# Kernel optimization log

Hardware: AMD Instinct MI355X
Metric: run time of the kernel (lower is better)

Reference implementation:

```python
import jax, jax.numpy as jnp
import numpy as np
from itertools import combinations

WIRES, LAYERS, CUTOFF, OUT_WIRES, BATCH = 4, 2, 10, 3, 2048

def _annih(c):
    # annihilation operator a in the Fock basis, truncated to cutoff c
    return jnp.diag(jnp.sqrt(jnp.arange(1, c, dtype=jnp.float32)), 1).astype(jnp.complex64)

_expm = jnp.vectorize(jax.scipy.linalg.expm, signature='(n,n)->(n,n)')

def _squeeze(r, phi, a):
    # S(z) = exp((z* a^2 - z a+^2)/2), z = r e^{i phi}; r, phi have arbitrary batch shape
    z = (r * jnp.exp(1j * phi)).astype(jnp.complex64)[..., None, None]
    a2 = a @ a
    ad2 = a.conj().T @ a.conj().T
    return _expm(0.5 * (jnp.conj(z) * a2 - z * ad2))

def _disp(r, phi, a):
    # D(alpha) = exp(alpha a+ - alpha* a), alpha = r e^{i phi}
    al = (r * jnp.exp(1j * phi)).astype(jnp.complex64)[..., None, None]
    ad = a.conj().T
    return _expm(al * ad - jnp.conj(al) * a)

def _bs(theta, phi, a):
    # SF BSgate: B = exp(theta (e^{i phi} a b+ - e^{-i phi} a+ b))
    ad = a.conj().T
    G = theta * (jnp.exp(1j * phi) * jnp.kron(a, ad) - jnp.exp(-1j * phi) * jnp.kron(ad, a))
    return jax.scipy.linalg.expm(G.astype(jnp.complex64))

def _cx(s, a):
    # SF CXgate: exp(-i s x1 p2 / hbar) = exp(-(s/2) (a+a+) kron (b-b+)) with hbar=2
    ad = a.conj().T
    G = (-s / 2.0) * jnp.kron(a + ad, a - ad)
    return jax.scipy.linalg.expm(G.astype(jnp.complex64))

def _apply1(state, U, m):
    # apply single-mode gate U ([c,c] shared or [B,c,c] per-sample) to mode m
    if U.ndim == 2:
        return jnp.moveaxis(jnp.tensordot(state, U, axes=[[1 + m], [1]]), -1, 1 + m)
    st = jnp.moveaxis(state, 1 + m, -1)
    st = jnp.einsum('b...j,bij->b...i', st, U)
    return jnp.moveaxis(st, -1, 1 + m)

def _apply2(state, U4, m1, m2):
    # apply two-mode gate U4 [c,c,c,c] (out1,out2,in1,in2) to modes (m1, m2)
    st = jnp.moveaxis(state, (1 + m1, 1 + m2), (-2, -1))
    st = jnp.einsum('b...kl,ijkl->b...ij', st, U4)
    return jnp.moveaxis(st, (-2, -1), (1 + m1, 1 + m2))

def _forward(jets, s_scale, disp_mag, disp_phase, squeeze_mag, squeeze_phase, w_dense, b_dense):
    B, c = jets.shape[0], CUTOFF
    a = _annih(c)
    eta, phi, pt = jets[:, :, 0], jets[:, :, 1], jets[:, :, 2]  # each [B, WIRES]
    scale = 10.0 / (1.0 + jnp.exp(-s_scale)) + 0.01
    # vacuum |0...0> for every sample
    state = jnp.zeros((B,) + (c,) * WIRES, jnp.complex64)
    state = state.at[(slice(None),) + (0,) * WIRES].set(1.0)
    # per-sample data-encoding gates
    S_enc = _squeeze(eta, pt * phi / 2.0, a)      # [B, WIRES, c, c]
    D_enc = _disp(scale * pt, eta, a)             # [B, WIRES, c, c]
    for w in range(WIRES):
        state = _apply1(state, S_enc[:, w], w)
        state = _apply1(state, D_enc[:, w], w)
    # fixed entangling gates (shared across batch)
    CX = _cx(1.0, a).reshape(c, c, c, c)
    BS = _bs(jnp.pi / 4.0, jnp.pi / 2.0, a).reshape(c, c, c, c)
    # learned per-layer single-mode gates (shared across batch)
    S_lay = _squeeze(squeeze_mag, squeeze_phase, a)  # [LAYERS, WIRES, c, c]
    D_lay = _disp(disp_mag, disp_phase, a)
    for L in range(LAYERS):
        for (i, j) in combinations(range(WIRES), 2):
            state = _apply2(state, CX, i, j)
        for i in range(WIRES):
            state = _apply2(state, BS, i, (i + 1) % WIRES)
        for w in range(WIRES):
            state = _apply1(state, S_lay[L, w], w)
            state = _apply1(state, D_lay[L, w], w)
    probs = jnp.abs(state) ** 2
    nvec = jnp.arange(c, dtype=jnp.float32)
    photons = jnp.stack(
        [probs.sum(axis=tuple(1 + k for k in range(WIRES) if k != m)) @ nvec
         for m in range(OUT_WIRES)], axis=1)  # [B, OUT_WIRES] mean photon numbers
    return (photons @ w_dense + b_dense)[:, 0]  # [B]

def setup_inputs() -> dict:
    key = jax.random.key(0)
    ks = jax.random.split(key, 8)
    u = lambda k, sh: jax.random.uniform(k, sh, jnp.float32, -1.0, 1.0)
    return {
        'jets': 0.3 * jax.random.normal(ks[0], (BATCH, WIRES, 3), jnp.float32),
        's_scale': u(ks[1], ()),
        'disp_mag': u(ks[2], (LAYERS, WIRES)),
        'disp_phase': u(ks[3], (LAYERS, WIRES)),
        'squeeze_mag': u(ks[4], (LAYERS, WIRES)),
        'squeeze_phase': u(ks[5], (LAYERS, WIRES)),
        'w_dense': u(ks[6], (OUT_WIRES, 1)),
        'b_dense': jnp.zeros((1,), jnp.float32),
    }

def reference(jets, s_scale, disp_mag, disp_phase, squeeze_mag, squeeze_phase, w_dense, b_dense):
    return _forward(jets, s_scale, disp_mag, disp_phase, squeeze_mag, squeeze_phase, w_dense, b_dense)
```

## Files before the change

### kernel.cpp

```cpp
#include <hip/hip_runtime.h>
#include <math.h>


namespace {

constexpr int NTB = 1024;
constexpr int SMEM_STATE = 162352;
constexpr double THETA = 0.7853981633974483096;

struct cxf { float x, y; };
typedef float v2f __attribute__((ext_vector_type(2)));
typedef float v4f __attribute__((ext_vector_type(4)));

constexpr int U_OFF = 15872;

__device__ __forceinline__ cxf gen_squeeze_f(int i, int j, float zr, float zi){
  if (j == i+2){ float g = 0.5f*sqrtf((float)((i+1)*(i+2))); return {zr*g, -zi*g}; }
  if (i == j+2){ float g = 0.5f*sqrtf((float)((j+1)*(j+2))); return {-zr*g, -zi*g}; }
  return {0.f, 0.f};
}
__device__ __forceinline__ cxf gen_disp_f(int i, int j, float ar, float ai){
  if (i == j+1){ float g = sqrtf((float)i); return {ar*g, ai*g}; }
  if (j == i+1){ float g = sqrtf((float)j); return {-ar*g, ai*g}; }
  return {0.f, 0.f};
}

__device__ void expm_f32(bool act, int n, cxf* M, cxf* P, cxf* T, cxf* R, int lane){
  const int n2 = n*n;
  if (act){
    for (int e=lane; e<n2; e+=64){ M[e].x *= 0x1p-10f; M[e].y *= 0x1p-10f; }
    for (int e=lane; e<n2; e+=64){
      P[e] = M[e];
      cxf r = M[e];
      if (e % (n+1) == 0) r.x += 1.f;
      R[e] = r;
    }
  }
  __syncthreads();
  for (int t=2; t<=12; ++t){
    if (act){
      float inv = 1.f/(float)t;
      for (int e=lane; e<n2; e+=64){
        int i = e/n, j = e - i*n;
        float ax=0.f, ay=0.f;
        for (int k=0;k<n;k++){
          cxf p = P[i*n+k], m = M[k*n+j];
          ax += p.x*m.x - p.y*m.y;
          ay += p.x*m.y + p.y*m.x;
        }
        T[e] = {ax*inv, ay*inv};
      }
    }
    __syncthreads();
    { cxf* tmp = P; P = T; T = tmp; }
    if (act){ for (int e=lane; e<n2; e+=64){ R[e].x += P[e].x; R[e].y += P[e].y; } }
    __syncthreads();
  }
  for (int s=0; s<10; ++s){
    if (act){
      for (int e=lane; e<n2; e+=64){
        int i = e/n, j = e - i*n;
        float ax=0.f, ay=0.f;
        for (int k=0;k<n;k++){
          cxf p = R[i*n+k], q = R[k*n+j];
          ax += p.x*q.x - p.y*q.y;
          ay += p.x*q.y + p.y*q.x;
        }
        T[e] = {ax, ay};
      }
    }
    __syncthreads();
    { cxf* tmp = R; R = T; T = tmp; }
    __syncthreads();
  }
}

__global__ __launch_bounds__(256)
void gates_kernel(const float* __restrict__ dmag, const float* __restrict__ dphase,
                  const float* __restrict__ smag, const float* __restrict__ sphase,
                  float* __restrict__ wsf){
  __shared__ double lam[10];
  __shared__ float scr[4][4][200];
  const int tid = threadIdx.x;
  const int wv = tid >> 6, lane = tid & 63, g = blockIdx.x;
  float* ws_V  = wsf;
  float* ws_VT = wsf + 100;
  float* ws_W  = wsf + 200;
  cxf* ws_BS   = (cxf*)(wsf + 1200);
  cxf* ws_stage= (cxf*)(wsf + 6600);

  if (tid < 10){
    double lo = -6.0, hi = 6.0;
    for (int it=0; it<80; ++it){
      double mid = 0.5*(lo+hi);
      int cnt = 0; double q = 1.0;
      for (int i=0;i<10;i++){
        q = -mid - (i ? (double)i/q : 0.0);
        if (fabs(q) < 1e-300) q = -1e-300;
        if (q < 0.0) cnt++;
      }
      if (cnt > tid) hi = mid; else lo = mid;
    }
    double x = 0.5*(lo+hi);
    double p[10];
    p[0] = 1.0; p[1] = x;
    for (int k=1;k<9;k++) p[k+1] = (x*p[k] - sqrt((double)k)*p[k-1]) * (1.0/sqrt((double)(k+1)));
    double nn=0.0; for (int k=0;k<10;k++) nn += p[k]*p[k];
    double inv = 1.0/sqrt(nn);
    lam[tid] = x;
    if (g == 0){
      for (int k=0;k<10;k++){
        float v = (float)(p[k]*inv);
        ws_V[k*10+tid]  = v;
        ws_VT[tid*10+k] = v;
      }
    }
  }
  __syncthreads();

  int t = g*4 + wv;
  bool act = (t < 45);
  int n = 10, bn = 0, ilo = 0;
  if (act && t >= 10 && t < 29){
    bn = t - 10; ilo = bn < 10 ? 0 : bn - 9;
    int ihi = bn < 10 ? bn : 9;
    n = ihi - ilo + 1;
  }
  cxf* M = (cxf*)scr[wv][0];
  cxf* P = (cxf*)scr[wv][1];
  cxf* T = (cxf*)scr[wv][2];
  cxf* R = (cxf*)scr[wv][3];
  if (act){
    if (t < 10){
      float l = (float)lam[t];
      for (int e=lane; e<100; e+=64){
        int i=e/10, j=e-10*i;
        float v = 0.f;
        if (j == i+1) v = -0.5f*l*sqrtf((float)(i+1));
        else if (i == j+1) v = 0.5f*l*sqrtf((float)i);
        M[e] = {v, 0.f};
      }
    } else if (t < 29){
      for (int e=lane; e<n*n; e+=64){
        int rr=e/n, c=e-n*rr;
        float v = 0.f;
        if (c == rr+1) v = (float)THETA*sqrtf((float)((ilo+rr+1)*(bn-ilo-rr)));
        else if (rr == c+1) v = (float)THETA*sqrtf((float)((ilo+c+1)*(bn-ilo-c)));
        M[e] = {0.f, v};
      }
    } else {
      int idx = t-29, kind = idx>>3, L=(idx>>2)&1, w=idx&3;
      float r_ = kind ? dmag[L*4+w]   : smag[L*4+w];
      float ph = kind ? dphase[L*4+w] : sphase[L*4+w];
      float zr = r_*cosf(ph), zi = r_*sinf(ph);
      for (int e=lane; e<100; e+=64){
        int i=e/10, j=e-10*i;
        M[e] = kind ? gen_disp_f(i,j,zr,zi) : gen_squeeze_f(i,j,zr,zi);
      }
    }
  }
  __syncthreads();
  expm_f32(act, n, M, P, T, R, lane);
  if (act){
    if (t < 10){
      for (int e=lane;e<100;e+=64){
        int i=e/10, j=e-10*i;
        ws_W[t*100 + j*10 + i] = R[e].x;
      }
    } else if (t < 29){
      for (int e=lane;e<100;e+=64){
        int rr=e/10, c=e-10*rr;
        cxf o; o.x=0.f; o.y=0.f;
        if (rr < n && c < n) o = R[rr*n+c];
        ws_BS[bn*100 + c*10 + rr] = o;
      }
    } else {
      int idx = t-29;
      for (int e=lane;e<100;e+=64) ws_stage[idx*100 + e] = R[e];
    }
  }
}

__global__ __launch_bounds__(512)
void fuse_kernel(float* __restrict__ wsf){
  __shared__ cxf ulraw[8][100];
  const int tid = threadIdx.x, wv = tid>>6, lane = tid&63;
  const cxf* stage = (const cxf*)(wsf + 6600);
  cxf* ws_UL = (cxf*)(wsf + 5000);
  cxf* ws_WU = (cxf*)(wsf + 9800);
  const float* V  = wsf;
  const float* Wt = wsf + 200;
  const cxf* Sm = stage + wv*100;
  const cxf* Dm = stage + (8+wv)*100;
  for (int e=lane; e<100; e+=64){
    int i=e/10, j=e-10*i;
    float ax=0.f, ay=0.f;
    for (int k=0;k<10;k++){
      cxf d=Dm[i*10+k], s=Sm[k*10+j];
      ax += d.x*s.x - d.y*s.y;
      ay += d.x*s.y + d.y*s.x;
    }
    ulraw[wv][e] = {ax, ay};
  }
  __syncthreads();
  cxf t0={0.f,0.f}, t1={0.f,0.f};
  if (wv == 0){
    {
      int e=lane, i=e/10, j=e-10*i;
      float ox=0.f, oy=0.f;
      for (int k=0;k<10;k++){ float v=V[k*10+i]; ox+=v*ulraw[0][k*10+j].x; oy+=v*ulraw[0][k*10+j].y; }
      t0 = {ox, oy};
    }
    if (lane+64 < 100){
      int e=lane+64, i=e/10, j=e-10*i;
      float ox=0.f, oy=0.f;
      for (int k=0;k<10;k++){ float v=V[k*10+i]; ox+=v*ulraw[0][k*10+j].x; oy+=v*ulraw[0][k*10+j].y; }
      t1 = {ox, oy};
    }
  }
  __syncthreads();
  if (wv == 0){
    ulraw[0][lane] = t0;
    if (lane+64 < 100) ulraw[0][lane+64] = t1;
  }
  __syncthreads();
  for (int e=tid; e<400; e+=512){
    int fi = e/100, r = e-100*fi;
    int f = (fi==0) ? 0 : (3+fi);
    int i=r/10, j=r-10*i;
    ws_UL[f*100 + j*10 + i] = ulraw[f][i*10+j];
  }
  for (int round=0; round<4; ++round){
    int id = round*8 + wv;
    if (id < 30){
      int b = 1 + id/10, n = id - (id/10)*10;
      const cxf* Ub = ulraw[b];
      for (int e=lane; e<100; e+=64){
        int i=e/10, j=e-10*i;
        float ax=0.f, ay=0.f;
        for (int k=0;k<10;k++){
          float w = Wt[n*100 + k*10 + i];
          ax += w*Ub[k*10+j].x;
          ay += w*Ub[k*10+j].y;
        }
        cxf o; o.x=ax; o.y=ay;
        ws_WU[id*100 + j*10 + i] = o;
      }
    }
  }
}

__global__ __launch_bounds__(128)
void enc_kernel(const float* __restrict__ jets, const float* __restrict__ sscale,
                float* __restrict__ wsf){
  __shared__ float scr[2][4][200];
  __shared__ cxf col[10];
  __shared__ cxf uacc[10];
  const int tid = threadIdx.x, wv = tid>>6, lane = tid&63;
  const int blk = blockIdx.x, b = blk>>2, w = blk&3;

  float eta = jets[b*12 + w*3 + 0];
  float jph = jets[b*12 + w*3 + 1];
  float pt  = jets[b*12 + w*3 + 2];

  cxf* M = (cxf*)scr[wv][0];
  cxf* P = (cxf*)scr[wv][1];
  cxf* T = (cxf*)scr[wv][2];
  cxf* R = (cxf*)scr[wv][3];
  {
    float zr, zi;
    if (wv == 0){ float phs = pt*jph*0.5f; zr = eta*cosf(phs); zi = eta*sinf(phs); }
    else {
      double sc = 10.0/(1.0 + exp(-(double)sscale[0])) + 0.01;
      float mag = (float)sc*pt; zr = mag*cosf(eta); zi = mag*sinf(eta);
    }
    for (int e=lane; e<100; e+=64){
      int i=e/10, j=e-10*i;
      M[e] = wv ? gen_disp_f(i,j,zr,zi) : gen_squeeze_f(i,j,zr,zi);
    }
  }
  __syncthreads();
  expm_f32(true, 10, M, P, T, R, lane);
  cxf* Rs = (cxf*)scr[0][3];
  cxf* Rd = (cxf*)scr[1][3];
  if (tid < 10) col[tid] = Rs[tid*10];
  __syncthreads();
  if (tid < 10){
    float ax=0.f, ay=0.f;
    for (int k=0;k<10;k++){
      cxf d = Rd[tid*10+k], c = col[k];
      ax += d.x*c.x - d.y*c.y;
      ay += d.x*c.y + d.y*c.x;
    }
    uacc[tid] = {ax, ay};
  }
  __syncthreads();
  if (tid < 10){
    float rx, ry;
    if (w == 0){
      rx = 0.f; ry = 0.f;
      for (int k=0;k<10;k++){
        float v = wsf[k*10 + tid];
        rx += v*uacc[k].x;
        ry += v*uacc[k].y;
      }
    } else { rx = uacc[tid].x; ry = uacc[tid].y; }
    float* u_out = wsf + U_OFF + (b*40 + w*10 + tid)*2;
    u_out[0] = rx;
    u_out[1] = ry;
  }
}

__device__ __forceinline__ constexpr int WS(int w){
  return w==0 ? 1010 : (w==1 ? 101 : (w==2 ? 10 : 1));
}

#define DECL_ACC4 \
  v4f a0={0.f,0.f,0.f,0.f}, a1=a0, a2=a0, a3=a0, a4=a0, \
      a5=a0, a6=a0, a7=a0, a8=a0, a9=a0;

#define LDS_RD10 \
  v4f r0=S[base], r1=S[base+sm], r2=S[base+2*sm], r3=S[base+3*sm], r4=S[base+4*sm], \
      r5=S[base+5*sm], r6=S[base+6*sm], r7=S[base+7*sm], r8=S[base+8*sm], r9=S[base+9*sm];

#define CE(i,ur,ui) \
  a##i = __builtin_elementwise_fma((v4f){(ur),(ur),(ur),(ur)}, vv, a##i); \
  a##i = __builtin_elementwise_fma((v4f){-(ui),(ui),-(ui),(ui)}, vs, a##i);
#define RE(i,u) a##i = __builtin_elementwise_fma((v4f){(u),(u),(u),(u)}, vv, a##i);

#define CSTEP(rk,krow) { \
  const v4f* Up = (const v4f*)(U + (krow)*10); \
  v4f q0=Up[0],q1=Up[1],q2=Up[2],q3=Up[3],q4=Up[4]; \
  v4f vv=rk, vs=__builtin_shufflevector(rk,rk,1,0,3,2); \
  CE(0,q0.x,q0.y) CE(1,q0.z,q0.w) CE(2,q1.x,q1.y) CE(3,q1.z,q1.w) \
  CE(4,q2.x,q2.y) CE(5,q2.z,q2.w) CE(6,q3.x,q3.y) CE(7,q3.z,q3.w) \
  CE(8,q4.x,q4.y) CE(9,q4.z,q4.w) }
#define CSTEP_ALL CSTEP(r0,0) CSTEP(r1,1) CSTEP(r2,2) CSTEP(r3,3) CSTEP(r4,4) \
  CSTEP(r5,5) CSTEP(r6,6) CSTEP(r7,7) CSTEP(r8,8) CSTEP(r9,9)

#define RSTEP2(ra_,rb_,krow) { \
  const v4f* Mp = (const v4f*)(Mt + (krow)*10); \
  v4f q0=Mp[0],q1=Mp[1],q2=Mp[2],q3=Mp[3],q4=Mp[4]; \
  { v4f vv=ra_; RE(0,q0.x) RE(1,q0.y) RE(2,q0.z) RE(3,q0.w) RE(4,q1.x) \
                RE(5,q1.y) RE(6,q1.z) RE(7,q1.w) RE(8,q2.x) RE(9,q2.y) } \
  { v4f vv=rb_; RE(0,q2.z) RE(1,q2.w) RE(2,q3.x) RE(3,q3.y) RE(4,q3.z) \
                RE(5,q3.w) RE(6,q4.x) RE(7,q4.y) RE(8,q4.z) RE(9,q4.w) } }
#define RSTEP_ALL RSTEP2(r0,r1,0) RSTEP2(r2,r3,2) RSTEP2(r4,r5,4) \
  RSTEP2(r6,r7,6) RSTEP2(r8,r9,8)

#define PST4(i) { S[base + (i)*sm] = a##i; }
#define PALL4 PST4(0) PST4(1) PST4(2) PST4(3) PST4(4) PST4(5) PST4(6) PST4(7) PST4(8) PST4(9)
#define BSTQ(r) if ((r) < sz){ S[wadr] = a##r; wadr += ds; }
#define BSTQ_ALL BSTQ(0) BSTQ(1) BSTQ(2) BSTQ(3) BSTQ(4) BSTQ(5) BSTQ(6) BSTQ(7) BSTQ(8) BSTQ(9)

__device__ __forceinline__ void apply1_c4(v4f* S, const cxf* __restrict__ U, int m, int tid){
  const int sm = WS(m);
  const int x0 = (m==0)?1:0, x1=(m<=1)?2:1, x2=(m<=2)?3:2;
  const int s0 = WS(x0), s1 = WS(x1), s2 = WS(x2);
  if (tid < 1000){
    int c0=tid/100, rem=tid-100*c0, c1=rem/10, c2=rem-10*c1;
    int base = c0*s0 + c1*s1 + c2*s2;
    LDS_RD10
    DECL_ACC4
    CSTEP_ALL
    PALL4
  }
}

__device__ __forceinline__ void apply1_r4(v4f* S, const float* __restrict__ Mt, int m, int tid){
  const int sm = WS(m);
  const int x0 = (m==0)?1:0, x1=(m<=1)?2:1, x2=(m<=2)?3:2;
  const int s0 = WS(x0), s1 = WS(x1), s2 = WS(x2);
  if (tid < 1000){
    int c0=tid/100, rem=tid-100*c0, c1=rem/10, c2=rem-10*c1;
    int base = c0*s0 + c1*s1 + c2*s2;
    LDS_RD10
    DECL_ACC4
    RSTEP_ALL
    PALL4
  }
}

__device__ __forceinline__ void applyW4(v4f* S, const float* __restrict__ Wall, int m1, int m2, int tid){
  const int sm  = WS(m2);
  const int sm1 = WS(m1);
  int ra=-1, rb=-1;
  for (int q=0;q<4;q++) if (q!=m1 && q!=m2){ if (ra<0) ra=q; else rb=q; }
  const int sa0 = WS(ra), sb0 = WS(rb);
  const bool sw = (sa0==101 && sb0==10);
  const int sa = sw ? sb0 : sa0, sb = sw ? sa0 : sb0;
  if (tid < 1000){
    int n = tid/100, rem = tid-100*n, qa = rem/10, qb = rem-10*qa;
    int base = n*sm1 + qa*sa + qb*sb;
    const float* __restrict__ Mt = Wall + n*100;
    LDS_RD10
    DECL_ACC4
    RSTEP_ALL
    PALL4
  }
}

__device__ __forceinline__ void applyWU4(v4f* S, const cxf* __restrict__ WUall, int m2, int tid){
  const int sm = WS(m2);
  const int ra = (m2==1)?2:1;
  const int rb = (m2==3)?2:3;
  const int sa0 = WS(ra), sb0 = WS(rb);
  const bool sw = (sa0==101 && sb0==10);
  const int sa = sw ? sb0 : sa0, sb = sw ? sa0 : sb0;
  if (tid < 1000){
    int n = tid/100, rem = tid-100*n, qa = rem/10, qb = rem-10*qa;
    int base = n*WS(0) + qa*sa + qb*sb;
    const cxf* __restrict__ U = WUall + n*100;
    LDS_RD10
    DECL_ACC4
    CSTEP_ALL
    PALL4
  }
}

__device__ __forceinline__ v2f measure14(const v4f* S, const cxf* __restrict__ U, int m, int tid){
  const int sm = WS(m);
  const int x0 = (m==0)?1:0, x1=(m<=1)?2:1, x2=3;
  const int s0 = WS(x0), s1 = WS(x1), s2 = WS(x2);
  v2f s = {0.f, 0.f};
  if (tid < 1000){
    int c0=tid/100, rem=tid-100*c0, c1=rem/10, c2=rem-10*c1;
    int base = c0*s0 + c1*s1 + c2*s2;
    LDS_RD10
    DECL_ACC4
    CSTEP_ALL
    #define MQ4(i) { s.x += (float)(i)*(a##i.x*a##i.x + a##i.y*a##i.y); \
                     s.y += (float)(i)*(a##i.z*a##i.z + a##i.w*a##i.w); }
    MQ4(1) MQ4(2) MQ4(3) MQ4(4) MQ4(5) MQ4(6) MQ4(7) MQ4(8) MQ4(9)
    #undef MQ4
  }
  return s;
}

__device__ __forceinline__ void applyBS4(v4f* S, const cxf* __restrict__ BSp, int m1, int m2, int tid){
  int ra=-1, rb=-1;
  for (int q=0;q<4;q++) if (q!=m1 && q!=m2){ if (ra<0) ra=q; else rb=q; }
  const int sa0 = WS(ra), sb0 = WS(rb);
  const bool sw = (sa0==101 && sb0==10);
  const int sa = sw ? sb0 : sa0, sb = sw ? sa0 : sb0;
  const int s1 = WS(m1), s2 = WS(m2);
  const int ds = s1 - s2;
  #pragma unroll 1
  for (int w0=0; w0<2048; w0+=NTB){
    int it = w0 + tid;
    if (it < 1900){
      int bn = it/100, rest = it-100*bn;
      int ilo = bn<10?0:bn-9, ihi = bn<10?bn:9, sz = ihi-ilo+1;
      int ca = rest/10, cb = rest-10*ca;
      int base = ca*sa + cb*sb;
      const cxf* __restrict__ Bt = BSp + bn*100;
      DECL_ACC4
      int radr = base + ilo*s1 + (bn-ilo)*s2;
      int kk = 0;
      #pragma unroll 1
      for (int c=0;c<sz;c++){
        v4f vv = S[radr];
        v4f vs = __builtin_shufflevector(vv, vv, 1, 0, 3, 2);
        const v4f* Bp = (const v4f*)(Bt + kk);
        v4f q0=Bp[0],q1=Bp[1],q2=Bp[2],q3=Bp[3],q4=Bp[4];
        CE(0,q0.x,q0.y) CE(1,q0.z,q0.w) CE(2,q1.x,q1.y) CE(3,q1.z,q1.w)
        CE(4,q2.x,q2.y) CE(5,q2.z,q2.w) CE(6,q3.x,q3.y) CE(7,q3.z,q3.w)
        CE(8,q4.x,q4.y) CE(9,q4.z,q4.w)
        radr += ds; kk += 10;
      }
      int wadr = base + ilo*s1 + (bn-ilo)*s2;
      BSTQ_ALL
    }
  }
}

__global__ __launch_bounds__(NTB)
__attribute__((amdgpu_waves_per_eu(4)))
void state_kernel(const float* __restrict__ wd, const float* __restrict__ bd,
                  const float* __restrict__ wsf, float* __restrict__ out){
  extern __shared__ __align__(16) char smem[];
  v4f* S    = (v4f*)smem;
  cxf* uv   = (cxf*)(smem + 161584);
  v2f* red  = (v2f*)(smem + 162224);

  const float* __restrict__ V   = wsf;
  const float* __restrict__ VT  = wsf + 100;
  const float* __restrict__ W   = wsf + 200;
  const cxf*   __restrict__ BSm = (const cxf*)(wsf + 1200);
  const cxf*   __restrict__ UL  = (const cxf*)(wsf + 5000);
  const cxf*   __restrict__ WU  = (const cxf*)(wsf + 9800);
  const cxf*   __restrict__ uw  = (const cxf*)(wsf + U_OFF);

  const int tid = threadIdx.x, wv = tid>>6, lane = tid&63;
  const int b = blockIdx.x;

  if (tid < 80) uv[tid] = uw[b*80 + tid];
  __syncthreads();

  for (int e=tid; e<10000; e+=NTB){
    int c0=e/1000, r_=e-1000*c0, c1=r_/100, r2_=r_-100*c1, c2=r2_/10, c3=r2_-10*c2;
    cxf A0 = uv[c0],    B0 = uv[10+c1], C0 = uv[20+c2], D0 = uv[30+c3];
    cxf A1 = uv[40+c0], B1 = uv[50+c1], C1 = uv[60+c2], D1 = uv[70+c3];
    float pr = A0.x*B0.x - A0.y*B0.y, pi = A0.x*B0.y + A0.y*B0.x;
    float qr = pr*C0.x - pi*C0.y,  qi = pr*C0.y + pi*C0.x;
    float e0r = qr*D0.x - qi*D0.y, e0i = qr*D0.y + qi*D0.x;
    pr = A1.x*B1.x - A1.y*B1.y; pi = A1.x*B1.y + A1.y*B1.x;
    qr = pr*C1.x - pi*C1.y;  qi = pr*C1.y + pi*C1.x;
    float e1r = qr*D1.x - qi*D1.y, e1i = qr*D1.y + qi*D1.x;
    S[c0*1010 + c1*101 + c2*10 + c3] = (v4f){e0r, e0i, e1r, e1i};
  }
  __syncthreads();

  applyW4(S, W, 0, 1, tid); __syncthreads();
  applyW4(S, W, 0, 2, tid); __syncthreads();
  applyW4(S, W, 0, 3, tid); __syncthreads();
  apply1_r4(S, VT, 0, tid); __syncthreads();
  apply1_r4(S, V, 1, tid);  __syncthreads();
  applyW4(S, W, 1, 2, tid); __syncthreads();
  applyW4(S, W, 1, 3, tid); __syncthreads();
  apply1_r4(S, VT, 1, tid); __syncthreads();
  apply1_r4(S, V, 2, tid);  __syncthreads();
  applyW4(S, W, 2, 3, tid); __syncthreads();
  apply1_r4(S, VT, 2, tid); __syncthreads();
  applyBS4(S, BSm, 0, 1, tid); __syncthreads();
  applyBS4(S, BSm, 1, 2, tid); __syncthreads();
  applyBS4(S, BSm, 2, 3, tid); __syncthreads();
  applyBS4(S, BSm, 3, 0, tid); __syncthreads();
  apply1_c4(S, UL, 0, tid); __syncthreads();

  applyWU4(S, WU,        1, tid); __syncthreads();
  applyWU4(S, WU + 1000, 2, tid); __syncthreads();
  applyWU4(S, WU + 2000, 3, tid); __syncthreads();
  apply1_r4(S, VT, 0, tid); __syncthreads();
  apply1_r4(S, V, 1, tid);  __syncthreads();
  applyW4(S, W, 1, 2, tid); __syncthreads();
  applyW4(S, W, 1, 3, tid); __syncthreads();
  apply1_r4(S, VT, 1, tid); __syncthreads();
  apply1_r4(S, V, 2, tid);  __syncthreads();
  applyW4(S, W, 2, 3, tid); __syncthreads();
  apply1_r4(S, VT, 2, tid); __syncthreads();
  applyBS4(S, BSm, 0, 1, tid); __syncthreads();
  applyBS4(S, BSm, 1, 2, tid); __syncthreads();
  applyBS4(S, BSm, 2, 3, tid); __syncthreads();
  applyBS4(S, BSm, 3, 0, tid); __syncthreads();

  float w0 = wd[0], w1 = wd[1], w2 = wd[2];
  v2f m0 = measure14(S, UL + 400, 0, tid);
  v2f m1 = measure14(S, UL + 500, 1, tid);
  v2f m2 = measure14(S, UL + 600, 2, tid);
  v2f acc;
  acc.x = w0*m0.x + w1*m1.x + w2*m2.x;
  acc.y = w0*m0.y + w1*m1.y + w2*m2.y;

  for (int off=32; off; off>>=1){
    acc.x += __shfl_down(acc.x, off, 64);
    acc.y += __shfl_down(acc.y, off, 64);
  }
  if (lane == 0) red[wv] = acc;
  __syncthreads();
  if (tid == 0){
    float sx = 0.f, sy = 0.f;
    for (int i=0;i<16;i++){ sx += red[i].x; sy += red[i].y; }
    out[2*b+0] = sx + bd[0];
    out[2*b+1] = sy + bd[0];
  }
}

}

extern "C" void kernel_launch(void* const* d_in, const int* in_sizes, int n_in,
                              void* d_out, int out_size, void* d_ws, size_t ws_size,
                              hipStream_t stream){
  const float* jets   = (const float*)d_in[0];
  const float* sscale = (const float*)d_in[1];
  const float* dmag   = (const float*)d_in[2];
  const float* dphase = (const float*)d_in[3];
  const float* smag   = (const float*)d_in[4];
  const float* sphase = (const float*)d_in[5];
  const float* wd     = (const float*)d_in[6];
  const float* bd     = (const float*)d_in[7];
  float* out = (float*)d_out;
  float* wsf = (float*)d_ws;
  int B = in_sizes[0] / 12;

  (void)hipFuncSetAttribute(reinterpret_cast<const void*>(&state_kernel),
                            hipFuncAttributeMaxDynamicSharedMemorySize, SMEM_STATE);

  gates_kernel<<<12, 256, 0, stream>>>(dmag, dphase, smag, sphase, wsf);
  fuse_kernel<<<1, 512, 0, stream>>>(wsf);
  enc_kernel<<<B*4, 128, 0, stream>>>(jets, sscale, wsf);
  state_kernel<<<B/2, NTB, SMEM_STATE, stream>>>(wd, bd, wsf, out);
}
```

Measured before the change: 860.8 us.

## Fuse consecutive diagonal-weighted gates on the same mode line into register passes

Chains of CX-style weighted gates and single-mode V transforms that act along the same mode are fused, so one thread applies two or three 10x10 stages in registers before writing back. This removes several LDS read/write passes and block barriers per layer, and reorders the gate sequence to group same-mode operations. It raises register pressure, with three sets of ten v4f accumulators live at once, which could cause spills or lower occupancy. It also relies on the reordered gates commuting as assumed.

```diff
diff --git a/kernel.cpp b/kernel.cpp
--- a/kernel.cpp
+++ b/kernel.cpp
@@ -315,106 +315,165 @@
   return w==0 ? 1010 : (w==1 ? 101 : (w==2 ? 10 : 1));
 }
 
-#define DECL_ACC4 \
-  v4f a0={0.f,0.f,0.f,0.f}, a1=a0, a2=a0, a3=a0, a4=a0, \
-      a5=a0, a6=a0, a7=a0, a8=a0, a9=a0;
+#define DECLP(P) v4f P##0={0.f,0.f,0.f,0.f}, P##1=P##0, P##2=P##0, P##3=P##0, \
+  P##4=P##0, P##5=P##0, P##6=P##0, P##7=P##0, P##8=P##0, P##9=P##0;
+
+#define REX(O,i,u) O##i = __builtin_elementwise_fma((v4f){(u),(u),(u),(u)}, vv, O##i);
+
+#define RPAIRX(O, va, vb, Mp_) { \
+  const v4f* Mp = (Mp_); \
+  v4f q0=Mp[0],q1=Mp[1],q2=Mp[2],q3=Mp[3],q4=Mp[4]; \
+  { v4f vv=va; REX(O,0,q0.x) REX(O,1,q0.y) REX(O,2,q0.z) REX(O,3,q0.w) REX(O,4,q1.x) \
+               REX(O,5,q1.y) REX(O,6,q1.z) REX(O,7,q1.w) REX(O,8,q2.x) REX(O,9,q2.y) } \
+  { v4f vv=vb; REX(O,0,q2.z) REX(O,1,q2.w) REX(O,2,q3.x) REX(O,3,q3.y) REX(O,4,q3.z) \
+               REX(O,5,q3.w) REX(O,6,q4.x) REX(O,7,q4.y) REX(O,8,q4.z) REX(O,9,q4.w) } }
+
+#define RSTAGE(Mt, I, O) \
+  RPAIRX(O, I##0, I##1, (const v4f*)((Mt)+0))  \
+  RPAIRX(O, I##2, I##3, (const v4f*)((Mt)+20)) \
+  RPAIRX(O, I##4, I##5, (const v4f*)((Mt)+40)) \
+  RPAIRX(O, I##6, I##7, (const v4f*)((Mt)+60)) \
+  RPAIRX(O, I##8, I##9, (const v4f*)((Mt)+80))
+
+#define CEX(O,i,ur,ui) \
+  O##i = __builtin_elementwise_fma((v4f){(ur),(ur),(ur),(ur)}, vv, O##i); \
+  O##i = __builtin_elementwise_fma((v4f){-(ui),(ui),-(ui),(ui)}, vs, O##i);
+
+#define CROWX(O, vk, Up_) { \
+  const v4f* Up = (Up_); \
+  v4f q0=Up[0],q1=Up[1],q2=Up[2],q3=Up[3],q4=Up[4]; \
+  v4f vv=vk, vs=__builtin_shufflevector(vk,vk,1,0,3,2); \
+  CEX(O,0,q0.x,q0.y) CEX(O,1,q0.z,q0.w) CEX(O,2,q1.x,q1.y) CEX(O,3,q1.z,q1.w) \
+  CEX(O,4,q2.x,q2.y) CEX(O,5,q2.z,q2.w) CEX(O,6,q3.x,q3.y) CEX(O,7,q3.z,q3.w) \
+  CEX(O,8,q4.x,q4.y) CEX(O,9,q4.z,q4.w) }
+
+#define CSTAGE(U, I, O) \
+  CROWX(O, I##0, (const v4f*)((U)+0))  CROWX(O, I##1, (const v4f*)((U)+10)) \
+  CROWX(O, I##2, (const v4f*)((U)+20)) CROWX(O, I##3, (const v4f*)((U)+30)) \
+  CROWX(O, I##4, (const v4f*)((U)+40)) CROWX(O, I##5, (const v4f*)((U)+50)) \
+  CROWX(O, I##6, (const v4f*)((U)+60)) CROWX(O, I##7, (const v4f*)((U)+70)) \
+  CROWX(O, I##8, (const v4f*)((U)+80)) CROWX(O, I##9, (const v4f*)((U)+90))
 
 #define LDS_RD10 \
   v4f r0=S[base], r1=S[base+sm], r2=S[base+2*sm], r3=S[base+3*sm], r4=S[base+4*sm], \
       r5=S[base+5*sm], r6=S[base+6*sm], r7=S[base+7*sm], r8=S[base+8*sm], r9=S[base+9*sm];
 
-#define CE(i,ur,ui) \
-  a##i = __builtin_elementwise_fma((v4f){(ur),(ur),(ur),(ur)}, vv, a##i); \
-  a##i = __builtin_elementwise_fma((v4f){-(ui),(ui),-(ui),(ui)}, vs, a##i);
-#define RE(i,u) a##i = __builtin_elementwise_fma((v4f){(u),(u),(u),(u)}, vv, a##i);
-
-#define CSTEP(rk,krow) { \
-  const v4f* Up = (const v4f*)(U + (krow)*10); \
-  v4f q0=Up[0],q1=Up[1],q2=Up[2],q3=Up[3],q4=Up[4]; \
-  v4f vv=rk, vs=__builtin_shufflevector(rk,rk,1,0,3,2); \
-  CE(0,q0.x,q0.y) CE(1,q0.z,q0.w) CE(2,q1.x,q1.y) CE(3,q1.z,q1.w) \
-  CE(4,q2.x,q2.y) CE(5,q2.z,q2.w) CE(6,q3.x,q3.y) CE(7,q3.z,q3.w) \
-  CE(8,q4.x,q4.y) CE(9,q4.z,q4.w) }
-#define CSTEP_ALL CSTEP(r0,0) CSTEP(r1,1) CSTEP(r2,2) CSTEP(r3,3) CSTEP(r4,4) \
-  CSTEP(r5,5) CSTEP(r6,6) CSTEP(r7,7) CSTEP(r8,8) CSTEP(r9,9)
-
-#define RSTEP2(ra_,rb_,krow) { \
-  const v4f* Mp = (const v4f*)(Mt + (krow)*10); \
-  v4f q0=Mp[0],q1=Mp[1],q2=Mp[2],q3=Mp[3],q4=Mp[4]; \
-  { v4f vv=ra_; RE(0,q0.x) RE(1,q0.y) RE(2,q0.z) RE(3,q0.w) RE(4,q1.x) \
-                RE(5,q1.y) RE(6,q1.z) RE(7,q1.w) RE(8,q2.x) RE(9,q2.y) } \
-  { v4f vv=rb_; RE(0,q2.z) RE(1,q2.w) RE(2,q3.x) RE(3,q3.y) RE(4,q3.z) \
-                RE(5,q3.w) RE(6,q4.x) RE(7,q4.y) RE(8,q4.z) RE(9,q4.w) } }
-#define RSTEP_ALL RSTEP2(r0,r1,0) RSTEP2(r2,r3,2) RSTEP2(r4,r5,4) \
-  RSTEP2(r6,r7,6) RSTEP2(r8,r9,8)
-
-#define PST4(i) { S[base + (i)*sm] = a##i; }
-#define PALL4 PST4(0) PST4(1) PST4(2) PST4(3) PST4(4) PST4(5) PST4(6) PST4(7) PST4(8) PST4(9)
-#define BSTQ(r) if ((r) < sz){ S[wadr] = a##r; wadr += ds; }
-#define BSTQ_ALL BSTQ(0) BSTQ(1) BSTQ(2) BSTQ(3) BSTQ(4) BSTQ(5) BSTQ(6) BSTQ(7) BSTQ(8) BSTQ(9)
+#define PSTORE10(P) { S[base]=P##0; S[base+sm]=P##1; S[base+2*sm]=P##2; S[base+3*sm]=P##3; \
+  S[base+4*sm]=P##4; S[base+5*sm]=P##5; S[base+6*sm]=P##6; S[base+7*sm]=P##7; \
+  S[base+8*sm]=P##8; S[base+9*sm]=P##9; }
+
+__device__ __forceinline__ void fuse_w1_r(v4f* S, const float* __restrict__ Wall,
+                                          const float* __restrict__ Mu, int tid){
+  if (tid < 1000){
+    int d0=tid/100, rem=tid-100*d0, d1=rem/10, d2=rem-10*d1;
+    const int sm = 101;
+    int base = d0*1010 + d1*10 + d2;
+    LDS_RD10
+    const float* M1 = Wall + d0*100;
+    DECLP(a) RSTAGE(M1, r, a)
+    DECLP(b) RSTAGE(Mu, a, b)
+    PSTORE10(b)
+  }
+}
+__device__ __forceinline__ void fuse_w1_c(v4f* S, const cxf* __restrict__ WUb,
+                                          const float* __restrict__ Mu, int tid){
+  if (tid < 1000){
+    int d0=tid/100, rem=tid-100*d0, d1=rem/10, d2=rem-10*d1;
+    const int sm = 101;
+    int base = d0*1010 + d1*10 + d2;
+    LDS_RD10
+    const cxf* U1 = WUb + d0*100;
+    DECLP(a) CSTAGE(U1, r, a)
+    DECLP(b) RSTAGE(Mu, a, b)
+    PSTORE10(b)
+  }
+}
+__device__ __forceinline__ void fuse_w2_r(v4f* S, const float* __restrict__ Wall,
+                                          const float* __restrict__ Mu, int tid){
+  if (tid < 1000){
+    int d0=tid/100, rem=tid-100*d0, d1=rem/10, d2=rem-10*d1;
+    const int sm = 10;
+    int base = d0*1010 + d1*101 + d2;
+    LDS_RD10
+    const float* M1 = Wall + d0*100;
+    const float* M2 = Wall + d1*100;
+    DECLP(a) RSTAGE(M1, r, a)
+    DECLP(b) RSTAGE(M2, a, b)
+    DECLP(c) RSTAGE(Mu, b, c)
+    PSTORE10(c)
+  }
+}
+__device__ __forceinline__ void fuse_w2_c(v4f* S, const cxf* __restrict__ WUb,
+                                          const float* __restrict__ Wall,
+                                          const float* __restrict__ Mu, int tid){
+  if (tid < 1000){
+    int d0=tid/100, rem=tid-100*d0, d1=rem/10, d2=rem-10*d1;
+    const int sm = 10;
+    int base = d0*1010 + d1*101 + d2;
+    LDS_RD10
+    const cxf* U1 = WUb + d0*100;
+    const float* M2 = Wall + d1*100;
+    DECLP(a) CSTAGE(U1, r, a)
+    DECLP(b) RSTAGE(M2, a, b)
+    DECLP(c) RSTAGE(Mu, b, c)
+    PSTORE10(c)
+  }
+}
+__device__ __forceinline__ void fuse_w3_r(v4f* S, const float* __restrict__ Wall, int tid){
+  if (tid < 1000){
+    int d0=tid/100, rem=tid-100*d0, d1=rem/10, d2=rem-10*d1;
+    const int sm = 1;
+    int base = d0*1010 + d2*101 + d1*10;
+    LDS_RD10
+    const float* M1 = Wall + d0*100;
+    const float* M2 = Wall + d2*100;
+    const float* M3 = Wall + d1*100;
+    DECLP(a) RSTAGE(M1, r, a)
+    DECLP(b) RSTAGE(M2, a, b)
+    DECLP(c) RSTAGE(M3, b, c)
+    PSTORE10(c)
+  }
+}
+__device__ __forceinline__ void fuse_w3_c(v4f* S, const cxf* __restrict__ WUb,
+                                          const float* __restrict__ Wall, int tid){
+  if (tid < 1000){
+    int d0=tid/100, rem=tid-100*d0, d1=rem/10, d2=rem-10*d1;
+    const int sm = 1;
+    int base = d0*1010 + d2*101 + d1*10;
+    LDS_RD10
+    const cxf* U1 = WUb + d0*100;
+    const float* M2 = Wall + d2*100;
+    const float* M3 = Wall + d1*100;
+    DECLP(a) CSTAGE(U1, r, a)
+    DECLP(b) RSTAGE(M2, a, b)
+    DECLP(c) RSTAGE(M3, b, c)
+    PSTORE10(c)
+  }
+}
+
+__device__ __forceinline__ void apply1_r4(v4f* S, const float* __restrict__ Mt, int m, int tid){
+  const int sm = WS(m);
+  const int x0 = (m==0)?1:0, x1=(m<=1)?2:1, x2=(m<=2)?3:2;
+  const int s0 = WS(x0), s1 = WS(x1), s2 = WS(x2);
+  if (tid < 1000){
+    int d0=tid/100, rem=tid-100*d0, d1=rem/10, d2=rem-10*d1;
+    int base = d0*s0 + d1*s1 + d2*s2;
+    LDS_RD10
+    DECLP(a) RSTAGE(Mt, r, a)
+    PSTORE10(a)
+  }
+}
 
 __device__ __forceinline__ void apply1_c4(v4f* S, const cxf* __restrict__ U, int m, int tid){
   const int sm = WS(m);
   const int x0 = (m==0)?1:0, x1=(m<=1)?2:1, x2=(m<=2)?3:2;
   const int s0 = WS(x0), s1 = WS(x1), s2 = WS(x2);
   if (tid < 1000){
-    int c0=tid/100, rem=tid-100*c0, c1=rem/10, c2=rem-10*c1;
-    int base = c0*s0 + c1*s1 + c2*s2;
-    LDS_RD10
-    DECL_ACC4
-    CSTEP_ALL
-    PALL4
-  }
-}
-
-__device__ __forceinline__ void apply1_r4(v4f* S, const float* __restrict__ Mt, int m, int tid){
-  const int sm = WS(m);
-  const int x0 = (m==0)?1:0, x1=(m<=1)?2:1, x2=(m<=2)?3:2;
-  const int s0 = WS(x0), s1 = WS(x1), s2 = WS(x2);
-  if (tid < 1000){
-    int c0=tid/100, rem=tid-100*c0, c1=rem/10, c2=rem-10*c1;
-    int base = c0*s0 + c1*s1 + c2*s2;
-    LDS_RD10
-    DECL_ACC4
-    RSTEP_ALL
-    PALL4
-  }
-}
-
-__device__ __forceinline__ void applyW4(v4f* S, const float* __restrict__ Wall, int m1, int m2, int tid){
-  const int sm  = WS(m2);
-  const int sm1 = WS(m1);
-  int ra=-1, rb=-1;
-  for (int q=0;q<4;q++) if (q!=m1 && q!=m2){ if (ra<0) ra=q; else rb=q; }
-  const int sa0 = WS(ra), sb0 = WS(rb);
-  const bool sw = (sa0==101 && sb0==10);
-  const int sa = sw ? sb0 : sa0, sb = sw ? sa0 : sb0;
-  if (tid < 1000){
-    int n = tid/100, rem = tid-100*n, qa = rem/10, qb = rem-10*qa;
-    int base = n*sm1 + qa*sa + qb*sb;
-    const float* __restrict__ Mt = Wall + n*100;
-    LDS_RD10
-    DECL_ACC4
-    RSTEP_ALL
-    PALL4
-  }
-}
-
-__device__ __forceinline__ void applyWU4(v4f* S, const cxf* __restrict__ WUall, int m2, int tid){
-  const int sm = WS(m2);
-  const int ra = (m2==1)?2:1;
-  const int rb = (m2==3)?2:3;
-  const int sa0 = WS(ra), sb0 = WS(rb);
-  const bool sw = (sa0==101 && sb0==10);
-  const int sa = sw ? sb0 : sa0, sb = sw ? sa0 : sb0;
-  if (tid < 1000){
-    int n = tid/100, rem = tid-100*n, qa = rem/10, qb = rem-10*qa;
-    int base = n*WS(0) + qa*sa + qb*sb;
-    const cxf* __restrict__ U = WUall + n*100;
-    LDS_RD10
-    DECL_ACC4
-    CSTEP_ALL
-    PALL4
+    int d0=tid/100, rem=tid-100*d0, d1=rem/10, d2=rem-10*d1;
+    int base = d0*s0 + d1*s1 + d2*s2;
+    LDS_RD10
+    DECLP(a) CSTAGE(U, r, a)
+    PSTORE10(a)
   }
 }
 
@@ -424,11 +483,10 @@
   const int s0 = WS(x0), s1 = WS(x1), s2 = WS(x2);
   v2f s = {0.f, 0.f};
   if (tid < 1000){
-    int c0=tid/100, rem=tid-100*c0, c1=rem/10, c2=rem-10*c1;
-    int base = c0*s0 + c1*s1 + c2*s2;
-    LDS_RD10
-    DECL_ACC4
-    CSTEP_ALL
+    int d0=tid/100, rem=tid-100*d0, d1=rem/10, d2=rem-10*d1;
+    int base = d0*s0 + d1*s1 + d2*s2;
+    LDS_RD10
+    DECLP(a) CSTAGE(U, r, a)
     #define MQ4(i) { s.x += (float)(i)*(a##i.x*a##i.x + a##i.y*a##i.y); \
                      s.y += (float)(i)*(a##i.z*a##i.z + a##i.w*a##i.w); }
     MQ4(1) MQ4(2) MQ4(3) MQ4(4) MQ4(5) MQ4(6) MQ4(7) MQ4(8) MQ4(9)
@@ -437,6 +495,8 @@
   return s;
 }
 
+#define BSTQ(r) if ((r) < sz){ S[wadr] = a##r; wadr += ds; }
+#define BSTQ_ALL BSTQ(0) BSTQ(1) BSTQ(2) BSTQ(3) BSTQ(4) BSTQ(5) BSTQ(6) BSTQ(7) BSTQ(8) BSTQ(9)
 __device__ __forceinline__ void applyBS4(v4f* S, const cxf* __restrict__ BSp, int m1, int m2, int tid){
   int ra=-1, rb=-1;
   for (int q=0;q<4;q++) if (q!=m1 && q!=m2){ if (ra<0) ra=q; else rb=q; }
@@ -454,18 +514,13 @@
       int ca = rest/10, cb = rest-10*ca;
       int base = ca*sa + cb*sb;
       const cxf* __restrict__ Bt = BSp + bn*100;
-      DECL_ACC4
+      DECLP(a)
       int radr = base + ilo*s1 + (bn-ilo)*s2;
       int kk = 0;
       #pragma unroll 1
       for (int c=0;c<sz;c++){
-        v4f vv = S[radr];
-        v4f vs = __builtin_shufflevector(vv, vv, 1, 0, 3, 2);
-        const v4f* Bp = (const v4f*)(Bt + kk);
-        v4f q0=Bp[0],q1=Bp[1],q2=Bp[2],q3=Bp[3],q4=Bp[4];
-        CE(0,q0.x,q0.y) CE(1,q0.z,q0.w) CE(2,q1.x,q1.y) CE(3,q1.z,q1.w)
-        CE(4,q2.x,q2.y) CE(5,q2.z,q2.w) CE(6,q3.x,q3.y) CE(7,q3.z,q3.w)
-        CE(8,q4.x,q4.y) CE(9,q4.z,q4.w)
+        v4f rk = S[radr];
+        CROWX(a, rk, (const v4f*)(Bt + kk))
         radr += ds; kk += 10;
       }
       int wadr = base + ilo*s1 + (bn-ilo)*s2;
@@ -511,34 +566,24 @@
   }
   __syncthreads();
 
-  applyW4(S, W, 0, 1, tid); __syncthreads();
-  applyW4(S, W, 0, 2, tid); __syncthreads();
-  applyW4(S, W, 0, 3, tid); __syncthreads();
-  apply1_r4(S, VT, 0, tid); __syncthreads();
-  apply1_r4(S, V, 1, tid);  __syncthreads();
-  applyW4(S, W, 1, 2, tid); __syncthreads();
-  applyW4(S, W, 1, 3, tid); __syncthreads();
-  apply1_r4(S, VT, 1, tid); __syncthreads();
-  apply1_r4(S, V, 2, tid);  __syncthreads();
-  applyW4(S, W, 2, 3, tid); __syncthreads();
-  apply1_r4(S, VT, 2, tid); __syncthreads();
+  fuse_w1_r(S, W, V, tid);   __syncthreads();
+  fuse_w2_r(S, W, V, tid);   __syncthreads();
+  fuse_w3_r(S, W, tid);      __syncthreads();
+  apply1_r4(S, VT, 0, tid);  __syncthreads();
+  apply1_r4(S, VT, 1, tid);  __syncthreads();
+  apply1_r4(S, VT, 2, tid);  __syncthreads();
   applyBS4(S, BSm, 0, 1, tid); __syncthreads();
   applyBS4(S, BSm, 1, 2, tid); __syncthreads();
   applyBS4(S, BSm, 2, 3, tid); __syncthreads();
   applyBS4(S, BSm, 3, 0, tid); __syncthreads();
-  apply1_c4(S, UL, 0, tid); __syncthreads();
-
-  applyWU4(S, WU,        1, tid); __syncthreads();
-  applyWU4(S, WU + 1000, 2, tid); __syncthreads();
-  applyWU4(S, WU + 2000, 3, tid); __syncthreads();
-  apply1_r4(S, VT, 0, tid); __syncthreads();
-  apply1_r4(S, V, 1, tid);  __syncthreads();
-  applyW4(S, W, 1, 2, tid); __syncthreads();
-  applyW4(S, W, 1, 3, tid); __syncthreads();
-  apply1_r4(S, VT, 1, tid); __syncthreads();
-  apply1_r4(S, V, 2, tid);  __syncthreads();
-  applyW4(S, W, 2, 3, tid); __syncthreads();
-  apply1_r4(S, VT, 2, tid); __syncthreads();
+  apply1_c4(S, UL, 0, tid);  __syncthreads();
+
+  fuse_w1_c(S, WU,        V, tid); __syncthreads();
+  fuse_w2_c(S, WU + 1000, W, V, tid); __syncthreads();
+  fuse_w3_c(S, WU + 2000, W, tid); __syncthreads();
+  apply1_r4(S, VT, 0, tid);  __syncthreads();
+  apply1_r4(S, VT, 1, tid);  __syncthreads();
+  apply1_r4(S, VT, 2, tid);  __syncthreads();
   applyBS4(S, BSm, 0, 1, tid); __syncthreads();
   applyBS4(S, BSm, 1, 2, tid); __syncthreads();
   applyBS4(S, BSm, 2, 3, tid); __syncthreads();
```

New measurement: 845.8 us. No clear change (-1.7%).
